# Performance work log

Hardware: AMD Instinct MI355X
Metric: run time of the kernel (lower is better)

The kernel has to match this reference:

```python
import jax, jax.numpy as jnp
import numpy as np

V, E, H, L, B, T = 50000, 512, 512, 32, 64, 512


def _lstm_dir(xg, w_hh, reverse):
    # xg: [B,T,4H] precomputed input-to-gate projections (+ biases)
    b, t, g4 = xg.shape
    h_dim = g4 // 4
    def step(carry, xt):
        h, c = carry
        g = xt + h @ w_hh.T  # [B,4H], PyTorch gate order i,f,g,o
        i, f, gg, o = jnp.split(g, 4, axis=-1)
        c = jax.nn.sigmoid(f) * c + jax.nn.sigmoid(i) * jnp.tanh(gg)
        h = jax.nn.sigmoid(o) * jnp.tanh(c)
        return (h, c), h
    init = (jnp.zeros((b, h_dim), xg.dtype), jnp.zeros((b, h_dim), xg.dtype))
    _, hs = jax.lax.scan(step, init, jnp.swapaxes(xg, 0, 1), reverse=reverse)
    return jnp.swapaxes(hs, 0, 1)  # [B,T,H]


def _bilstm(x, w_ih0, w_ih1, w_hh, b_ih, b_hh):
    w_ihs = (w_ih0, w_ih1)
    for l in range(2):
        outs = []
        for d in range(2):  # 0=forward, 1=backward
            xg = jnp.einsum('bti,gi->btg', x, w_ihs[l][d]) + b_ih[l, d] + b_hh[l, d]
            outs.append(_lstm_dir(xg, w_hh[l, d], reverse=(d == 1)))
        x = jnp.concatenate(outs, axis=-1)  # [B,T,2H]
    return x


def _crf_nll(emissions, tags, start, end, trans):
    # pytorch-crf: returns sum log-likelihood; module returns its negation.
    emit = jnp.take_along_axis(emissions, tags[..., None], axis=-1)[..., 0]  # [B,T]
    num = (start[tags[:, 0]] + emit.sum(1)
           + trans[tags[:, :-1], tags[:, 1:]].sum(1) + end[tags[:, -1]])
    alpha0 = start + emissions[:, 0]  # [B,L]
    def step(alpha, e_t):
        s = alpha[:, :, None] + trans[None] + e_t[:, None, :]  # [B,L,L]
        return jax.nn.logsumexp(s, axis=1), None
    alpha, _ = jax.lax.scan(step, alpha0, jnp.swapaxes(emissions[:, 1:], 0, 1))
    denom = jax.nn.logsumexp(alpha + end, axis=-1)  # [B]
    return -(num - denom).sum()


def setup_inputs() -> dict:
    key = jax.random.key(0)
    ks = jax.random.split(key, 13)
    s = 0.05
    emb = jax.random.normal(ks[0], (V, E), jnp.float32) * s
    emb = emb.at[0].set(0.0)  # padding_idx=0
    return {
        'datas': jax.random.randint(ks[1], (B, T), 0, V, jnp.int32),
        'labels': jax.random.randint(ks[2], (B, T), 0, L, jnp.int32),
        'emb': emb,
        'w_ih0': jax.random.normal(ks[3], (2, 4 * H, E), jnp.float32) * s,
        'w_ih1': jax.random.normal(ks[4], (2, 4 * H, 2 * H), jnp.float32) * s,
        'w_hh': jax.random.normal(ks[5], (2, 2, 4 * H, H), jnp.float32) * s,
        'b_ih': jax.random.normal(ks[6], (2, 2, 4 * H), jnp.float32) * s,
        'b_hh': jax.random.normal(ks[7], (2, 2, 4 * H), jnp.float32) * s,
        'w_out': jax.random.normal(ks[8], (2 * H, L), jnp.float32) * s,
        'b_out': jax.random.normal(ks[9], (L,), jnp.float32) * s,
        'crf_start': jax.random.normal(ks[10], (L,), jnp.float32) * s,
        'crf_end': jax.random.normal(ks[11], (L,), jnp.float32) * s,
        'crf_trans': jax.random.normal(ks[12], (L, L), jnp.float32) * s,
    }


def reference(datas, labels, emb, w_ih0, w_ih1, w_hh, b_ih, b_hh, w_out, b_out,
              crf_start, crf_end, crf_trans):
    x = emb[datas]  # [B,T,E]
    h = _bilstm(x, w_ih0, w_ih1, w_hh, b_ih, b_hh)  # [B,T,2H]; dropout=0 (eval)
    emissions = h @ w_out + b_out  # [B,T,L]
    return _crf_nll(emissions, labels, crf_start, crf_end, crf_trans)
```

## Files before the change

### kernel.cpp

```cpp
#include <hip/hip_runtime.h>

typedef unsigned short ushort_t;
typedef unsigned long long u64_t;
typedef __attribute__((ext_vector_type(8))) short short8;
typedef __attribute__((ext_vector_type(4))) float floatx4;


__device__ __forceinline__ float bf2f(ushort_t u) {
  unsigned x = ((unsigned)u) << 16;
  return __builtin_bit_cast(float, x);
}
__device__ __forceinline__ ushort_t f2bf(float f) {
  unsigned x = __builtin_bit_cast(unsigned, f);
  x += 0x7FFFu + ((x >> 16) & 1u);
  return (ushort_t)(x >> 16);
}
__device__ __forceinline__ float sigf(float x) { return 1.0f / (1.0f + __expf(-x)); }
__device__ __forceinline__ float tanhf_(float x) { return 1.0f - 2.0f / (__expf(2.0f * x) + 1.0f); }

static const size_t OFF_A    = 0;
static const size_t OFF_OUT0 = 67108864;
static const size_t OFF_XG   = 134217728;
static const size_t OFF_WIH0 = 167772160;
static const size_t OFF_WIH1 = 171966464;
static const size_t OFF_BIAS = 180355072;
static const size_t OFF_WOUT = 180387840;
static const size_t OFF_HC   = 180453376;
static const size_t OFF_CST  = 181501952;
static const size_t OFF_BAR  = 182026240;
static const size_t OFF_NUM  = 182034432;
static const size_t OFF_PERB = 182034688;
static const size_t OFF_END  = 182034944;

__global__ void prep_kernel(const float* __restrict__ w_ih0, const float* __restrict__ w_ih1,
                            const float* __restrict__ b_ih, const float* __restrict__ b_hh,
                            const float* __restrict__ w_out,
                            ushort_t* __restrict__ wih0_bf, ushort_t* __restrict__ wih1_bf,
                            float* __restrict__ bias, ushort_t* __restrict__ wout_bf) {
  int idx = blockIdx.x * 256 + threadIdx.x;
  int stride = gridDim.x * 256;
  for (int i = idx; i < 2097152; i += stride) wih0_bf[i] = f2bf(w_ih0[i]);
  for (int i = idx; i < 4194304; i += stride) wih1_bf[i] = f2bf(w_ih1[i]);
  for (int i = idx; i < 8192; i += stride) bias[i] = b_ih[i] + b_hh[i];
  for (int i = idx; i < 32768; i += stride) {
    int j = i & 7, Ls = (i >> 3) & 63, kb = (i >> 9) & 31, nt = i >> 14;
    int n = nt * 16 + (Ls & 15);
    int k = kb * 32 + ((Ls >> 4) & 3) * 8 + j;
    wout_bf[i] = f2bf(w_out[k * 32 + n]);
  }
}

__global__ void embed_kernel(const int* __restrict__ datas, const float* __restrict__ emb,
                             ushort_t* __restrict__ x_bf) {
  int idx = blockIdx.x * 256 + threadIdx.x;
  int row = idx >> 6, sub = idx & 63;
  int tok = datas[row];
  const float4* ep = (const float4*)(emb + (size_t)tok * 512 + sub * 8);
  float4 f0 = ep[0], f1 = ep[1];
  short8 v;
  v[0] = (short)f2bf(f0.x); v[1] = (short)f2bf(f0.y);
  v[2] = (short)f2bf(f0.z); v[3] = (short)f2bf(f0.w);
  v[4] = (short)f2bf(f1.x); v[5] = (short)f2bf(f1.y);
  v[6] = (short)f2bf(f1.z); v[7] = (short)f2bf(f1.w);
  *(short8*)(x_bf + (size_t)row * 512 + sub * 8) = v;
}

__global__ __launch_bounds__(256) void gemm_chunk(const ushort_t* __restrict__ A, int K,
                                                  const ushort_t* __restrict__ W,
                                                  const float* __restrict__ biasL,
                                                  ushort_t* __restrict__ xg0c,
                                                  ushort_t* __restrict__ xg1c,
                                                  int t00, int t01) {
  __shared__ alignas(16) ushort_t alds[512 * 8];
  __shared__ alignas(16) ushort_t blds[512 * 8];
  int gid = blockIdx.x;
  int dir = gid >> 9, r = gid & 511;
  int mt = r & 31, ntt = r >> 5;
  int t0 = dir ? t01 : t00;
  const ushort_t* Bm = W + (size_t)dir * 2048 * K;
  const float* bptr = biasL + dir * 2048;
  ushort_t* xg = dir ? xg1c : xg0c;
  int bm0 = mt * 128, bn0 = ntt * 128;
  int tid = threadIdx.x, L = tid & 63, w = tid >> 6;
  int wm = w & 1, wn = w >> 1;
  floatx4 acc[4][4] = {};
  for (int k0 = 0; k0 < K; k0 += 32) {
    __syncthreads();
    #pragma unroll
    for (int rep = 0; rep < 2; rep++) {
      int slot = rep * 256 + tid;
      int t8 = slot >> 6, Ls = slot & 63;
      int col = k0 + (Ls >> 4) * 8;
      int mp = bm0 + t8 * 16 + (Ls & 15);
      int Arow = (mp >> 6) * 512 + t0 + (mp & 63);
      *(short8*)&alds[slot * 8] = *(const short8*)&A[(size_t)Arow * K + col];
      int rowb = bn0 + t8 * 16 + (Ls & 15);
      *(short8*)&blds[slot * 8] = *(const short8*)&Bm[(size_t)rowb * K + col];
    }
    __syncthreads();
    short8 af[4];
    #pragma unroll
    for (int a = 0; a < 4; a++) af[a] = *(const short8*)&alds[((wm * 4 + a) * 64 + L) * 8];
    #pragma unroll
    for (int bq = 0; bq < 4; bq++) {
      short8 bfr = *(const short8*)&blds[((wn * 4 + bq) * 64 + L) * 8];
      #pragma unroll
      for (int a = 0; a < 4; a++)
        acc[a][bq] = __builtin_amdgcn_mfma_f32_16x16x32_bf16(af[a], bfr, acc[a][bq], 0, 0, 0);
    }
  }
  int lm = L >> 4, ln = L & 15;
  #pragma unroll
  for (int bq = 0; bq < 4; bq++) {
    int n = bn0 + (wn * 4 + bq) * 16 + ln;
    float bv = bptr[n];
    #pragma unroll
    for (int a = 0; a < 4; a++) {
      #pragma unroll
      for (int rr = 0; rr < 4; rr++) {
        int m = bm0 + (wm * 4 + a) * 16 + lm * 4 + rr;
        int b = m >> 6, ts = m & 63;
        xg[((size_t)(ts * 64 + b)) * 2048 + n] = f2bf(acc[a][bq][rr] + bv);
      }
    }
  }
}

__global__ __launch_bounds__(256) void lstm_chunk(const ushort_t* __restrict__ xg0c,
                                                  const ushort_t* __restrict__ xg1c,
                                                  const float* __restrict__ whh_f,
                                                  ushort_t* __restrict__ hcL,
                                                  float* __restrict__ cstL,
                                                  ushort_t* __restrict__ outL,
                                                  int* __restrict__ barF, int c) {
  __shared__ alignas(16) ushort_t wlds[32768];
  int bid = blockIdx.x, d = bid >> 5, g = bid & 31, j0 = g * 16;
  int tid = threadIdx.x, L = tid & 63, w = tid >> 6;
  const float* wptr = whh_f + (size_t)d * 2048 * 512;
  #pragma unroll
  for (int it = 0; it < 16; it++) {
    int slot = it * 256 + tid;
    int q = slot >> 10, kb = (slot >> 6) & 15, Ls = slot & 63;
    int gcol = q * 512 + j0 + (Ls & 15);
    int k = kb * 32 + (Ls >> 4) * 8;
    const float* src = wptr + (size_t)gcol * 512 + k;
    float4 f0 = *(const float4*)src;
    float4 f1 = *(const float4*)(src + 4);
    short8 v;
    v[0] = (short)f2bf(f0.x); v[1] = (short)f2bf(f0.y);
    v[2] = (short)f2bf(f0.z); v[3] = (short)f2bf(f0.w);
    v[4] = (short)f2bf(f1.x); v[5] = (short)f2bf(f1.y);
    v[6] = (short)f2bf(f1.z); v[7] = (short)f2bf(f1.w);
    *(short8*)&wlds[slot * 8] = v;
  }
  __syncthreads();
  const ushort_t* xgd = d ? xg1c : xg0c;
  ushort_t* hcd = hcL + (size_t)d * 2 * 32768;
  int* flg = barF + d * 512;
  int* myflag = flg + g * 16;
  int q8 = L >> 4, jj = L & 15;
  int mbase = w * 16 + q8 * 4;
  int wslot = ((w * 16 + (g >> 1)) * 64 + q8 * 4 + 16 * ((g & 1) * 2 + (jj >> 3))) * 8 + (jj & 7);
  int rbase = (w * 16 * 64 + L) * 8;
  float cv[4];
  #pragma unroll
  for (int rr = 0; rr < 4; rr++) cv[rr] = cstL[(size_t)d * 32768 + (mbase + rr) * 512 + j0 + jj];

  auto ldxg = [&](int sl2, ushort_t dst[4][4]) {
    int ts2 = d ? (63 - sl2) : sl2;
    #pragma unroll
    for (int rr = 0; rr < 4; rr++) {
      const ushort_t* xrow = xgd + ((size_t)(ts2 * 64 + mbase + rr)) * 2048 + j0 + jj;
      #pragma unroll
      for (int q = 0; q < 4; q++) dst[q][rr] = xrow[q * 512];
    }
  };

  ushort_t xgu[4][4];
  ldxg(0, xgu);

  for (int sl = 0; sl < 64; sl++) {
    int s = c * 64 + sl;
    int t = d ? (511 - s) : s;
    const u64_t* h64 = (const u64_t*)(hcd + (size_t)(s & 1) * 32768);
    unsigned* h32w = (unsigned*)(hcd + (size_t)((s + 1) & 1) * 32768);
    int b64 = rbase >> 2;
    u64_t hv[32];
    #pragma unroll
    for (int kb = 0; kb < 16; kb++) {
      hv[2 * kb]     = __hip_atomic_load(h64 + b64 + kb * 128,     __ATOMIC_RELAXED, __HIP_MEMORY_SCOPE_SYSTEM);
      hv[2 * kb + 1] = __hip_atomic_load(h64 + b64 + kb * 128 + 1, __ATOMIC_RELAXED, __HIP_MEMORY_SCOPE_SYSTEM);
    }
    floatx4 acc[4] = {};
    #pragma unroll
    for (int kb = 0; kb < 16; kb++) {
      union { u64_t u[2]; short8 v; } pk;
      pk.u[0] = hv[2 * kb];
      pk.u[1] = hv[2 * kb + 1];
      short8 a = pk.v;
      #pragma unroll
      for (int q = 0; q < 4; q++) {
        short8 bfr = *(const short8*)&wlds[((q * 16 + kb) * 64 + L) * 8];
        acc[q] = __builtin_amdgcn_mfma_f32_16x16x32_bf16(a, bfr, acc[q], 0, 0, 0);
      }
    }
    ushort_t hbv[4];
    #pragma unroll
    for (int rr = 0; rr < 4; rr++) {
      float ii = acc[0][rr] + bf2f(xgu[0][rr]);
      float ff = acc[1][rr] + bf2f(xgu[1][rr]);
      float gg = acc[2][rr] + bf2f(xgu[2][rr]);
      float oo = acc[3][rr] + bf2f(xgu[3][rr]);
      float cc = sigf(ff) * cv[rr] + sigf(ii) * tanhf_(gg);
      cv[rr] = cc;
      hbv[rr] = f2bf(sigf(oo) * tanhf_(cc));
    }
    bool evn = (jj & 1) == 0;
    unsigned pk4[4];
    #pragma unroll
    for (int rr = 0; rr < 4; rr++) {
      unsigned mine = (unsigned)hbv[rr];
      unsigned nb = (unsigned)__shfl_xor((int)mine, 1, 64);
      pk4[rr] = mine | (nb << 16);
      if (evn)
        __hip_atomic_store(h32w + ((wslot + rr * 8) >> 1), pk4[rr],
                           __ATOMIC_RELAXED, __HIP_MEMORY_SCOPE_SYSTEM);
    }
    if (sl != 63) {
      asm volatile("s_waitcnt vmcnt(0)" ::: "memory");
      __builtin_amdgcn_s_barrier();
      asm volatile("" ::: "memory");
      if (tid == 0)
        __hip_atomic_store(myflag, s + 1, __ATOMIC_RELAXED, __HIP_MEMORY_SCOPE_SYSTEM);
      if (evn) {
        #pragma unroll
        for (int rr = 0; rr < 4; rr++) {
          int m = mbase + rr;
          *(unsigned*)&outL[((size_t)m * 512 + t) * 1024 + (d << 9) + j0 + jj] = pk4[rr];
        }
      }
      ldxg(sl + 1, xgu);
      if (tid < 64) {
        int target = s + 1, guard = 0;
        while (guard < (1 << 17)) {
          int f = __hip_atomic_load(flg + (tid & 31) * 16, __ATOMIC_RELAXED, __HIP_MEMORY_SCOPE_SYSTEM);
          if (__ballot(f >= target) == ~0ULL) break;
          guard++;
        }
      }
      __builtin_amdgcn_s_barrier();
      asm volatile("" ::: "memory");
    } else {
      if (evn) {
        #pragma unroll
        for (int rr = 0; rr < 4; rr++) {
          int m = mbase + rr;
          *(unsigned*)&outL[((size_t)m * 512 + t) * 1024 + (d << 9) + j0 + jj] = pk4[rr];
        }
      }
    }
  }
  #pragma unroll
  for (int rr = 0; rr < 4; rr++) cstL[(size_t)d * 32768 + (mbase + rr) * 512 + j0 + jj] = cv[rr];
}

__global__ __launch_bounds__(256) void emis_kernel(const ushort_t* __restrict__ out1,
                                                   const ushort_t* __restrict__ wout_bf,
                                                   const float* __restrict__ b_out,
                                                   float* __restrict__ emis) {
  int tid = threadIdx.x, L = tid & 63, w = tid >> 6;
  int bm0 = blockIdx.x * 128;
  int q8 = L >> 4, ln = L & 15;
  floatx4 acc[2][2] = {};
  #pragma unroll 4
  for (int kb = 0; kb < 32; kb++) {
    short8 a0 = *(const short8*)&out1[(size_t)(bm0 + (w * 2 + 0) * 16 + ln) * 1024 + kb * 32 + q8 * 8];
    short8 a1 = *(const short8*)&out1[(size_t)(bm0 + (w * 2 + 1) * 16 + ln) * 1024 + kb * 32 + q8 * 8];
    #pragma unroll
    for (int nt = 0; nt < 2; nt++) {
      short8 bfr = *(const short8*)&wout_bf[((size_t)(nt * 32 + kb) * 64 + L) * 8];
      acc[0][nt] = __builtin_amdgcn_mfma_f32_16x16x32_bf16(a0, bfr, acc[0][nt], 0, 0, 0);
      acc[1][nt] = __builtin_amdgcn_mfma_f32_16x16x32_bf16(a1, bfr, acc[1][nt], 0, 0, 0);
    }
  }
  #pragma unroll
  for (int mt = 0; mt < 2; mt++) {
    #pragma unroll
    for (int nt = 0; nt < 2; nt++) {
      int n = nt * 16 + ln;
      float bv = b_out[n];
      #pragma unroll
      for (int rr = 0; rr < 4; rr++) {
        int m = bm0 + (w * 2 + mt) * 16 + q8 * 4 + rr;
        emis[(size_t)m * 32 + n] = acc[mt][nt][rr] + bv;
      }
    }
  }
}

__global__ void num_kernel(const int* __restrict__ labels, const float* __restrict__ emis,
                           const float* __restrict__ trans, const float* __restrict__ cstart,
                           const float* __restrict__ cend, float* __restrict__ num) {
  int b = blockIdx.x, tid = threadIdx.x;
  float s = 0.f;
  for (int t = tid; t < 512; t += 64) {
    int tag = labels[b * 512 + t];
    s += emis[(size_t)(b * 512 + t) * 32 + tag];
    if (t < 511) s += trans[tag * 32 + labels[b * 512 + t + 1]];
  }
  #pragma unroll
  for (int off = 32; off > 0; off >>= 1) s += __shfl_xor(s, off, 64);
  if (tid == 0) num[b] = s + cstart[labels[b * 512]] + cend[labels[b * 512 + 511]];
}

__global__ __launch_bounds__(64) void fwd_kernel(const float* __restrict__ emis,
                                                 const float* __restrict__ trans,
                                                 const float* __restrict__ cstart,
                                                 const float* __restrict__ cend,
                                                 const float* __restrict__ num,
                                                 float* __restrict__ perb) {
  int b = blockIdx.x, tid = threadIdx.x, j = tid & 31;
  float etr[32];
  #pragma unroll
  for (int i = 0; i < 32; i++) etr[i] = __expf(trans[i * 32 + j]);
  float alpha = cstart[j] + emis[(size_t)(b * 512) * 32 + j];
  float e_cur = emis[(size_t)(b * 512 + 1) * 32 + j];
  for (int t = 1; t < 512; t++) {
    float e_nx = (t < 511) ? emis[(size_t)(b * 512 + t + 1) * 32 + j] : 0.f;
    float mA = alpha;
    mA = fmaxf(mA, __shfl_xor(mA, 1, 32));
    mA = fmaxf(mA, __shfl_xor(mA, 2, 32));
    mA = fmaxf(mA, __shfl_xor(mA, 4, 32));
    mA = fmaxf(mA, __shfl_xor(mA, 8, 32));
    mA = fmaxf(mA, __shfl_xor(mA, 16, 32));
    float p = __expf(alpha - mA);
    float s0 = 0.f, s1 = 0.f, s2 = 0.f, s3 = 0.f;
    #pragma unroll
    for (int i = 0; i < 32; i += 4) {
      s0 = fmaf(__shfl(p, i, 32),     etr[i],     s0);
      s1 = fmaf(__shfl(p, i + 1, 32), etr[i + 1], s1);
      s2 = fmaf(__shfl(p, i + 2, 32), etr[i + 2], s2);
      s3 = fmaf(__shfl(p, i + 3, 32), etr[i + 3], s3);
    }
    alpha = __logf((s0 + s1) + (s2 + s3)) + mA + e_cur;
    e_cur = e_nx;
  }
  float z = alpha + cend[j];
  float m2 = z;
  #pragma unroll
  for (int off = 16; off > 0; off >>= 1) m2 = fmaxf(m2, __shfl_xor(m2, off, 32));
  float s2r = __expf(z - m2);
  #pragma unroll
  for (int off = 16; off > 0; off >>= 1) s2r += __shfl_xor(s2r, off, 32);
  if (tid == 0) perb[b] = num[b] - (__logf(s2r) + m2);
}

__global__ void final_kernel(const float* __restrict__ perb, float* __restrict__ out) {
  int tid = threadIdx.x;
  float s = perb[tid];
  #pragma unroll
  for (int off = 32; off > 0; off >>= 1) s += __shfl_xor(s, off, 64);
  if (tid == 0) out[0] = -s;
}

extern "C" void kernel_launch(void* const* d_in, const int* in_sizes, int n_in,
                              void* d_out, int out_size, void* d_ws, size_t ws_size,
                              hipStream_t stream) {
  (void)in_sizes; (void)n_in; (void)out_size; (void)ws_size;
  const int* datas = (const int*)d_in[0];
  const int* labels = (const int*)d_in[1];
  const float* emb = (const float*)d_in[2];
  const float* w_ih0 = (const float*)d_in[3];
  const float* w_ih1 = (const float*)d_in[4];
  const float* w_hh = (const float*)d_in[5];
  const float* b_ih = (const float*)d_in[6];
  const float* b_hh = (const float*)d_in[7];
  const float* w_out = (const float*)d_in[8];
  const float* b_out = (const float*)d_in[9];
  const float* cstart = (const float*)d_in[10];
  const float* cend = (const float*)d_in[11];
  const float* ctrans = (const float*)d_in[12];

  char* ws = (char*)d_ws;
  ushort_t* x_bf = (ushort_t*)(ws + OFF_A);
  ushort_t* out1 = (ushort_t*)(ws + OFF_A);
  ushort_t* out0 = (ushort_t*)(ws + OFF_OUT0);
  ushort_t* xg0c = (ushort_t*)(ws + OFF_XG);
  ushort_t* xg1c = (ushort_t*)(ws + OFF_XG + 16777216);
  float* emis = (float*)(ws + OFF_XG);
  ushort_t* wih0_bf = (ushort_t*)(ws + OFF_WIH0);
  ushort_t* wih1_bf = (ushort_t*)(ws + OFF_WIH1);
  float* bias = (float*)(ws + OFF_BIAS);
  ushort_t* wout_bf = (ushort_t*)(ws + OFF_WOUT);
  ushort_t* hc0 = (ushort_t*)(ws + OFF_HC);
  ushort_t* hc1 = hc0 + 131072;
  float* cst0 = (float*)(ws + OFF_CST);
  float* cst1 = cst0 + 65536;
  int* bar = (int*)(ws + OFF_BAR);
  float* numb = (float*)(ws + OFF_NUM);
  float* perb = (float*)(ws + OFF_PERB);

  hipMemsetAsync(ws + OFF_HC, 0, OFF_END - OFF_HC, stream);

  prep_kernel<<<2048, 256, 0, stream>>>(w_ih0, w_ih1, b_ih, b_hh, w_out,
                                        wih0_bf, wih1_bf, bias, wout_bf);
  embed_kernel<<<8192, 256, 0, stream>>>(datas, emb, x_bf);

  for (int c = 0; c < 8; c++) {
    gemm_chunk<<<1024, 256, 0, stream>>>(x_bf, 512, wih0_bf, bias, xg0c, xg1c,
                                         c * 64, (7 - c) * 64);
    lstm_chunk<<<64, 256, 0, stream>>>(xg0c, xg1c, w_hh, hc0, cst0, out0, bar, c);
  }
  for (int c = 0; c < 8; c++) {
    gemm_chunk<<<1024, 256, 0, stream>>>(out0, 1024, wih1_bf, bias + 4096, xg0c, xg1c,
                                         c * 64, (7 - c) * 64);
    lstm_chunk<<<64, 256, 0, stream>>>(xg0c, xg1c, w_hh + 2097152, hc1, cst1, out1,
                                       bar + 1024, c);
  }

  emis_kernel<<<256, 256, 0, stream>>>(out1, wout_bf, b_out, emis);
  num_kernel<<<64, 64, 0, stream>>>(labels, emis, ctrans, cstart, cend, numb);
  fwd_kernel<<<64, 64, 0, stream>>>(emis, ctrans, cstart, cend, numb, perb);
  final_kernel<<<1, 64, 0, stream>>>(perb, (float*)d_out);
}
```

Baseline: 5.449 ms.

## Replace per-step flag barrier with sentinel-tagged 4-slot hidden-state ring

```diff
diff --git a/kernel.cpp b/kernel.cpp
--- a/kernel.cpp
+++ b/kernel.cpp
@@ -5,6 +5,9 @@
 typedef __attribute__((ext_vector_type(8))) short short8;
 typedef __attribute__((ext_vector_type(4))) float floatx4;
 
+
+#define SENT32 0x7FC07FC0u
+#define SENT64 0x7FC07FC07FC07FC0ULL
 
 __device__ __forceinline__ float bf2f(ushort_t u) {
   unsigned x = ((unsigned)u) << 16;
@@ -27,10 +30,9 @@
 static const size_t OFF_WOUT = 180387840;
 static const size_t OFF_HC   = 180453376;
 static const size_t OFF_CST  = 181501952;
-static const size_t OFF_BAR  = 182026240;
-static const size_t OFF_NUM  = 182034432;
-static const size_t OFF_PERB = 182034688;
-static const size_t OFF_END  = 182034944;
+static const size_t OFF_NUM  = 182026240;
+static const size_t OFF_PERB = 182026496;
+static const size_t OFF_END  = 182026752;
 
 __global__ void prep_kernel(const float* __restrict__ w_ih0, const float* __restrict__ w_ih1,
                             const float* __restrict__ b_ih, const float* __restrict__ b_hh,
@@ -47,6 +49,15 @@
     int n = nt * 16 + (Ls & 15);
     int k = kb * 32 + ((Ls >> 4) & 3) * 8 + j;
     wout_bf[i] = f2bf(w_out[k * 32 + n]);
+  }
+}
+
+__global__ void ring_init(unsigned* __restrict__ hc) {
+  int idx = blockIdx.x * 256 + threadIdx.x;
+  int total = 2 * 2 * 4 * 16384;
+  for (int i = idx; i < total; i += gridDim.x * 256) {
+    int buf = (i >> 14) & 3;
+    hc[i] = (buf == 0) ? 0u : SENT32;
   }
 }
 
@@ -132,7 +143,7 @@
                                                   ushort_t* __restrict__ hcL,
                                                   float* __restrict__ cstL,
                                                   ushort_t* __restrict__ outL,
-                                                  int* __restrict__ barF, int c) {
+                                                  int c) {
   __shared__ alignas(16) ushort_t wlds[32768];
   int bid = blockIdx.x, d = bid >> 5, g = bid & 31, j0 = g * 16;
   int tid = threadIdx.x, L = tid & 63, w = tid >> 6;
@@ -155,13 +166,12 @@
   }
   __syncthreads();
   const ushort_t* xgd = d ? xg1c : xg0c;
-  ushort_t* hcd = hcL + (size_t)d * 2 * 32768;
-  int* flg = barF + d * 512;
-  int* myflag = flg + g * 16;
+  ushort_t* hcd = hcL + (size_t)d * 4 * 32768;
   int q8 = L >> 4, jj = L & 15;
   int mbase = w * 16 + q8 * 4;
   int wslot = ((w * 16 + (g >> 1)) * 64 + q8 * 4 + 16 * ((g & 1) * 2 + (jj >> 3))) * 8 + (jj & 7);
   int rbase = (w * 16 * 64 + L) * 8;
+  int b64 = rbase >> 2;
   float cv[4];
   #pragma unroll
   for (int rr = 0; rr < 4; rr++) cv[rr] = cstL[(size_t)d * 32768 + (mbase + rr) * 512 + j0 + jj];
@@ -182,15 +192,33 @@
   for (int sl = 0; sl < 64; sl++) {
     int s = c * 64 + sl;
     int t = d ? (511 - s) : s;
-    const u64_t* h64 = (const u64_t*)(hcd + (size_t)(s & 1) * 32768);
-    unsigned* h32w = (unsigned*)(hcd + (size_t)((s + 1) & 1) * 32768);
-    int b64 = rbase >> 2;
+    const u64_t* hb = (const u64_t*)(hcd + (size_t)(s & 3) * 32768) + b64;
+    unsigned* h32w = (unsigned*)(hcd + (size_t)((s + 1) & 3) * 32768);
     u64_t hv[32];
     #pragma unroll
     for (int kb = 0; kb < 16; kb++) {
-      hv[2 * kb]     = __hip_atomic_load(h64 + b64 + kb * 128,     __ATOMIC_RELAXED, __HIP_MEMORY_SCOPE_SYSTEM);
-      hv[2 * kb + 1] = __hip_atomic_load(h64 + b64 + kb * 128 + 1, __ATOMIC_RELAXED, __HIP_MEMORY_SCOPE_SYSTEM);
-    }
+      hv[2 * kb]     = __hip_atomic_load(hb + kb * 128,     __ATOMIC_RELAXED, __HIP_MEMORY_SCOPE_AGENT);
+      hv[2 * kb + 1] = __hip_atomic_load(hb + kb * 128 + 1, __ATOMIC_RELAXED, __HIP_MEMORY_SCOPE_AGENT);
+    }
+    int guard = 0;
+    while (true) {
+      bool anybad = false;
+      #pragma unroll
+      for (int i = 0; i < 32; i++) {
+        unsigned lo = (unsigned)hv[i], hi = (unsigned)(hv[i] >> 32);
+        if (lo == SENT32 || hi == SENT32) anybad = true;
+      }
+      if (__ballot(anybad) == 0) break;
+      if (++guard > 8192) break;
+      #pragma unroll
+      for (int i = 0; i < 32; i++) {
+        unsigned lo = (unsigned)hv[i], hi = (unsigned)(hv[i] >> 32);
+        if (lo == SENT32 || hi == SENT32)
+          hv[i] = __hip_atomic_load(hb + (i >> 1) * 128 + (i & 1),
+                                    __ATOMIC_RELAXED, __HIP_MEMORY_SCOPE_AGENT);
+      }
+    }
+    asm volatile("s_waitcnt vmcnt(0)" ::: "memory");
     floatx4 acc[4] = {};
     #pragma unroll
     for (int kb = 0; kb < 16; kb++) {
@@ -224,41 +252,23 @@
       pk4[rr] = mine | (nb << 16);
       if (evn)
         __hip_atomic_store(h32w + ((wslot + rr * 8) >> 1), pk4[rr],
-                           __ATOMIC_RELAXED, __HIP_MEMORY_SCOPE_SYSTEM);
-    }
-    if (sl != 63) {
-      asm volatile("s_waitcnt vmcnt(0)" ::: "memory");
-      __builtin_amdgcn_s_barrier();
-      asm volatile("" ::: "memory");
-      if (tid == 0)
-        __hip_atomic_store(myflag, s + 1, __ATOMIC_RELAXED, __HIP_MEMORY_SCOPE_SYSTEM);
-      if (evn) {
-        #pragma unroll
-        for (int rr = 0; rr < 4; rr++) {
-          int m = mbase + rr;
-          *(unsigned*)&outL[((size_t)m * 512 + t) * 1024 + (d << 9) + j0 + jj] = pk4[rr];
-        }
-      }
-      ldxg(sl + 1, xgu);
-      if (tid < 64) {
-        int target = s + 1, guard = 0;
-        while (guard < (1 << 17)) {
-          int f = __hip_atomic_load(flg + (tid & 31) * 16, __ATOMIC_RELAXED, __HIP_MEMORY_SCOPE_SYSTEM);
-          if (__ballot(f >= target) == ~0ULL) break;
-          guard++;
-        }
-      }
-      __builtin_amdgcn_s_barrier();
-      asm volatile("" ::: "memory");
-    } else {
-      if (evn) {
-        #pragma unroll
-        for (int rr = 0; rr < 4; rr++) {
-          int m = mbase + rr;
-          *(unsigned*)&outL[((size_t)m * 512 + t) * 1024 + (d << 9) + j0 + jj] = pk4[rr];
-        }
-      }
-    }
+                           __ATOMIC_RELAXED, __HIP_MEMORY_SCOPE_AGENT);
+    }
+    asm volatile("" ::: "memory");
+    if (evn) {
+      #pragma unroll
+      for (int rr = 0; rr < 4; rr++) {
+        int m = mbase + rr;
+        *(unsigned*)&outL[((size_t)m * 512 + t) * 1024 + (d << 9) + j0 + jj] = pk4[rr];
+      }
+    }
+    if (sl != 63) ldxg(sl + 1, xgu);
+    if (g < 16) {
+      u64_t* rf = (u64_t*)(hcd + (size_t)((s + 3) & 3) * 32768) + b64 + g * 128;
+      __hip_atomic_store(rf,     SENT64, __ATOMIC_RELAXED, __HIP_MEMORY_SCOPE_AGENT);
+      __hip_atomic_store(rf + 1, SENT64, __ATOMIC_RELAXED, __HIP_MEMORY_SCOPE_AGENT);
+    }
+    asm volatile("" ::: "memory");
   }
   #pragma unroll
   for (int rr = 0; rr < 4; rr++) cstL[(size_t)d * 32768 + (mbase + rr) * 512 + j0 + jj] = cv[rr];
@@ -393,14 +403,14 @@
   float* bias = (float*)(ws + OFF_BIAS);
   ushort_t* wout_bf = (ushort_t*)(ws + OFF_WOUT);
   ushort_t* hc0 = (ushort_t*)(ws + OFF_HC);
-  ushort_t* hc1 = hc0 + 131072;
+  ushort_t* hc1 = hc0 + 262144;
   float* cst0 = (float*)(ws + OFF_CST);
   float* cst1 = cst0 + 65536;
-  int* bar = (int*)(ws + OFF_BAR);
   float* numb = (float*)(ws + OFF_NUM);
   float* perb = (float*)(ws + OFF_PERB);
 
-  hipMemsetAsync(ws + OFF_HC, 0, OFF_END - OFF_HC, stream);
+  hipMemsetAsync(ws + OFF_CST, 0, OFF_END - OFF_CST, stream);
+  ring_init<<<1024, 256, 0, stream>>>((unsigned*)(ws + OFF_HC));
 
   prep_kernel<<<2048, 256, 0, stream>>>(w_ih0, w_ih1, b_ih, b_hh, w_out,
                                         wih0_bf, wih1_bf, bias, wout_bf);
@@ -409,13 +419,12 @@
   for (int c = 0; c < 8; c++) {
     gemm_chunk<<<1024, 256, 0, stream>>>(x_bf, 512, wih0_bf, bias, xg0c, xg1c,
                                          c * 64, (7 - c) * 64);
-    lstm_chunk<<<64, 256, 0, stream>>>(xg0c, xg1c, w_hh, hc0, cst0, out0, bar, c);
+    lstm_chunk<<<64, 256, 0, stream>>>(xg0c, xg1c, w_hh, hc0, cst0, out0, c);
   }
   for (int c = 0; c < 8; c++) {
     gemm_chunk<<<1024, 256, 0, stream>>>(out0, 1024, wih1_bf, bias + 4096, xg0c, xg1c,
                                          c * 64, (7 - c) * 64);
-    lstm_chunk<<<64, 256, 0, stream>>>(xg0c, xg1c, w_hh + 2097152, hc1, cst1, out1,
-                                       bar + 1024, c);
+    lstm_chunk<<<64, 256, 0, stream>>>(xg0c, xg1c, w_hh + 2097152, hc1, cst1, out1, c);
   }
 
   emis_kernel<<<256, 256, 0, stream>>>(out1, wout_bf, b_out, emis);
```

After: 6.312 ms. 15.8% more time.
